# Optimization experiments

Measured on AMD Instinct MI355X. Metric: run time of the kernel, lower is better.

The kernel has to match this reference:

```python
import jax, jax.numpy as jnp
import numpy as np

N_NODES = 100000
N_EDGES = 1600000
F_IN = 128
F_OUT = 128


def _spmm(edge_row, edge_col, edge_weight, X):
    # sparse [N,N] @ dense [N,F]: gather source rows, weight, scatter-add to dest rows
    msgs = edge_weight[:, None] * X[edge_col]  # [E, F]
    return jax.ops.segment_sum(msgs, edge_row, num_segments=N_NODES)


def setup_inputs() -> dict:
    key = jax.random.key(0)
    ks = jax.random.split(key, 7)
    scale = 1.0 / np.sqrt(F_IN)
    return {
        "x": jax.random.normal(ks[0], (N_NODES, F_IN), dtype=jnp.float32),
        "edge_row": jax.random.randint(ks[1], (N_EDGES,), 0, N_NODES, dtype=jnp.int32),
        "edge_col": jax.random.randint(ks[2], (N_EDGES,), 0, N_NODES, dtype=jnp.int32),
        "edge_weight": jax.random.uniform(ks[3], (N_EDGES,), dtype=jnp.float32),
        "w1": jax.random.normal(ks[4], (F_IN, F_IN), dtype=jnp.float32) * scale,
        "w2": jax.random.normal(ks[5], (F_IN, F_OUT), dtype=jnp.float32) * scale,
        "w3": jax.random.normal(ks[6], (F_OUT, F_OUT), dtype=jnp.float32) * scale,
    }


def reference(x, edge_row, edge_col, edge_weight, w1, w2, w3):
    # dropout p=0.0 (eval) -> identity
    h = jax.nn.relu(_spmm(edge_row, edge_col, edge_weight, x @ w1))
    h = jax.nn.relu(_spmm(edge_row, edge_col, edge_weight, h @ w2))
    h = jax.nn.relu(_spmm(edge_row, edge_col, edge_weight, h @ w3))
    return h
```

## Files before the change

### kernel.cpp

```cpp
#include <hip/hip_runtime.h>

#define N_NODES 100000
#define N_EDGES 1600000
#define F 128
#define XCD_RANGE 12500

#define SCAN_B 1024
#define SCAN_NB ((N_NODES + SCAN_B - 1) / SCAN_B)

typedef short bf16x8 __attribute__((ext_vector_type(8)));
typedef float f32x4  __attribute__((ext_vector_type(4)));
typedef unsigned int u32x4 __attribute__((ext_vector_type(4)));

union ABFrag {
    bf16x8 v;
    unsigned short u[8];
    u32x4  q;
};

__device__ __forceinline__ unsigned short f2bf(float f) {
    unsigned int u = __float_as_uint(f);
    u += 0x7fffu + ((u >> 16) & 1u);
    return (unsigned short)(u >> 16);
}
__device__ __forceinline__ float bflo(unsigned int u) {
    return __uint_as_float(u << 16);
}
__device__ __forceinline__ float bfhi(unsigned int u) {
    return __uint_as_float(u & 0xFFFF0000u);
}


__global__ __launch_bounds__(256) void edge_histogram_xcd(
    const int* __restrict__ erow, int* __restrict__ counts) {
    const int xcd = blockIdx.x & 7;
    const int e   = (blockIdx.x >> 3) * 256 + threadIdx.x;
    const int dst = erow[e];
    const int lo  = xcd * XCD_RANGE;
    if (dst >= lo && dst < lo + XCD_RANGE) {
        atomicAdd(&counts[dst], 1);
    }
}

__global__ void scan_block_sums(const int* __restrict__ counts, int* __restrict__ bsums) {
    __shared__ int s[SCAN_B];
    const int t = threadIdx.x;
    const int idx = blockIdx.x * SCAN_B + t;
    int v = (idx < N_NODES) ? counts[idx] : 0;
    s[t] = v;
    __syncthreads();
    for (int off = SCAN_B / 2; off > 0; off >>= 1) {
        if (t < off) s[t] += s[t + off];
        __syncthreads();
    }
    if (t == 0) bsums[blockIdx.x] = s[0];
}

__global__ void scan_bsums(const int* __restrict__ bsums, int* __restrict__ boffs) {
    __shared__ int s[128];
    const int t = threadIdx.x;
    int v = (t < SCAN_NB) ? bsums[t] : 0;
    s[t] = v;
    __syncthreads();
    for (int off = 1; off < 128; off <<= 1) {
        int u = (t >= off) ? s[t - off] : 0;
        __syncthreads();
        s[t] += u;
        __syncthreads();
    }
    if (t < SCAN_NB) boffs[t] = s[t] - v;
}

__global__ void scan_final(const int* __restrict__ counts, const int* __restrict__ boffs,
                           int* __restrict__ row_ptr) {
    __shared__ int s[SCAN_B];
    const int t = threadIdx.x;
    const int idx = blockIdx.x * SCAN_B + t;
    int v = (idx < N_NODES) ? counts[idx] : 0;
    s[t] = v;
    __syncthreads();
    for (int off = 1; off < SCAN_B; off <<= 1) {
        int u = (t >= off) ? s[t - off] : 0;
        __syncthreads();
        s[t] += u;
        __syncthreads();
    }
    if (idx < N_NODES) row_ptr[idx] = boffs[blockIdx.x] + s[t] - v;
    if (idx == 0) row_ptr[N_NODES] = N_EDGES;
}

__global__ __launch_bounds__(256) void csr_fill_xcd(
    const int* __restrict__ erow, const int* __restrict__ ecol,
    const float* __restrict__ ewgt,
    const int* __restrict__ row_ptr, int* __restrict__ cursor,
    unsigned int* __restrict__ pairs) {
    const int xcd = blockIdx.x & 7;
    const int e   = (blockIdx.x >> 3) * 256 + threadIdx.x;
    const int dst = erow[e];
    const int lo  = xcd * XCD_RANGE;
    if (dst >= lo && dst < lo + XCD_RANGE) {
        const int col = ecol[e];
        const float w = ewgt[e];
        const int pos = atomicAdd(&cursor[dst], 1);
        pairs[row_ptr[dst] + pos] = ((unsigned int)col << 15) | (unsigned int)f2bf(w);
    }
}

__global__ void transpose_w3(const float* __restrict__ w1, const float* __restrict__ w2,
                             const float* __restrict__ w3, unsigned short* __restrict__ wt) {
    const int i = blockIdx.x * 256 + threadIdx.x;
    const int which = i >> 14;
    const int j = i & 16383;
    const float* W = (which == 0) ? w1 : (which == 1) ? w2 : w3;
    const int n = j >> 7;
    const int k = j & 127;
    wt[i] = f2bf(W[k * F + n]);
}

__global__ __launch_bounds__(256) void gemm_mfma(
    const float* __restrict__ Xf,
    const unsigned short* __restrict__ Xb,
    const unsigned short* __restrict__ Wt,
    unsigned short* __restrict__ Y,
    int use_f32_in)
{
    __shared__ unsigned short Wl[4 * 8 * 64 * 8];

    const int tid  = threadIdx.x;
    const int wave = tid >> 6;
    const int lane = tid & 63;

    for (int s = tid; s < 2048; s += 256) {
        const int ln  = s & 63;
        const int ntk = s >> 6;
        const int nt  = ntk & 7;
        const int kt  = ntk >> 3;
        const int n   = nt * 16 + (ln & 15);
        const int k   = kt * 32 + (ln >> 4) * 8;
        *(u32x4*)(&Wl[s * 8]) = *(const u32x4*)(Wt + n * F + k);
    }
    __syncthreads();

    const int kq = (lane >> 4) * 8;
    const int m0 = blockIdx.x * 128 + wave * 16 + (lane & 15);
    const int m1 = m0 + 64;
    const bool v0 = (m0 < N_NODES);
    const bool v1 = (m1 < N_NODES);

    f32x4 acc[2][8] = {};

#pragma unroll
    for (int kt = 0; kt < 4; ++kt) {
        ABFrag a0, a1;
        a0.q = 0;
        a1.q = 0;
        if (use_f32_in) {
            if (v0) {
                const float* p = Xf + (size_t)m0 * F + kt * 32 + kq;
                const float4 u0 = *(const float4*)p;
                const float4 u1 = *(const float4*)(p + 4);
                a0.u[0] = f2bf(u0.x); a0.u[1] = f2bf(u0.y);
                a0.u[2] = f2bf(u0.z); a0.u[3] = f2bf(u0.w);
                a0.u[4] = f2bf(u1.x); a0.u[5] = f2bf(u1.y);
                a0.u[6] = f2bf(u1.z); a0.u[7] = f2bf(u1.w);
            }
            if (v1) {
                const float* p = Xf + (size_t)m1 * F + kt * 32 + kq;
                const float4 u0 = *(const float4*)p;
                const float4 u1 = *(const float4*)(p + 4);
                a1.u[0] = f2bf(u0.x); a1.u[1] = f2bf(u0.y);
                a1.u[2] = f2bf(u0.z); a1.u[3] = f2bf(u0.w);
                a1.u[4] = f2bf(u1.x); a1.u[5] = f2bf(u1.y);
                a1.u[6] = f2bf(u1.z); a1.u[7] = f2bf(u1.w);
            }
        } else {
            if (v0) {
                a0.q = *(const u32x4*)(Xb + (size_t)m0 * F + kt * 32 + kq);
#pragma unroll
                for (int j = 0; j < 8; ++j)
                    if (a0.u[j] & 0x8000u) a0.u[j] = 0;
            }
            if (v1) {
                a1.q = *(const u32x4*)(Xb + (size_t)m1 * F + kt * 32 + kq);
#pragma unroll
                for (int j = 0; j < 8; ++j)
                    if (a1.u[j] & 0x8000u) a1.u[j] = 0;
            }
        }
#pragma unroll
        for (int nt = 0; nt < 8; ++nt) {
            ABFrag b;
            b.q = *(const u32x4*)(&Wl[((kt * 8 + nt) * 64 + lane) * 8]);
            acc[0][nt] = __builtin_amdgcn_mfma_f32_16x16x32_bf16(a0.v, b.v, acc[0][nt], 0, 0, 0);
            acc[1][nt] = __builtin_amdgcn_mfma_f32_16x16x32_bf16(a1.v, b.v, acc[1][nt], 0, 0, 0);
        }
    }

    const int cbase = lane & 15;
#pragma unroll
    for (int t = 0; t < 2; ++t) {
        const int rbase = blockIdx.x * 128 + t * 64 + wave * 16 + (lane >> 4) * 4;
#pragma unroll
        for (int r = 0; r < 4; ++r) {
            const int row = rbase + r;
            if (row < N_NODES) {
#pragma unroll
                for (int nt = 0; nt < 8; ++nt) {
                    Y[(size_t)row * F + nt * 16 + cbase] = f2bf(acc[t][nt][r]);
                }
            }
        }
    }
}

__global__ __launch_bounds__(256) void spmm_csr_bf16(
    const unsigned short* __restrict__ Xb,
    const int* __restrict__ row_ptr,
    const unsigned int* __restrict__ pairs,
    unsigned short* __restrict__ Ob,
    float* __restrict__ Of,
    int final_mode) {
    const int tid = threadIdx.x;
    const int l16 = tid & 15;
    const int q   = tid >> 4;
    const int row = blockIdx.x * 16 + q;

    const int beg = row_ptr[row];
    const int end = row_ptr[row + 1];

    float a[8] = {};
    int i = beg;
    for (; i + 3 < end; i += 4) {
        const unsigned int p0 = __builtin_nontemporal_load(&pairs[i]);
        const unsigned int p1 = __builtin_nontemporal_load(&pairs[i + 1]);
        const unsigned int p2 = __builtin_nontemporal_load(&pairs[i + 2]);
        const unsigned int p3 = __builtin_nontemporal_load(&pairs[i + 3]);
        const u32x4 v0 = *(const u32x4*)(Xb + (size_t)(p0 >> 15) * F + l16 * 8);
        const u32x4 v1 = *(const u32x4*)(Xb + (size_t)(p1 >> 15) * F + l16 * 8);
        const u32x4 v2 = *(const u32x4*)(Xb + (size_t)(p2 >> 15) * F + l16 * 8);
        const u32x4 v3 = *(const u32x4*)(Xb + (size_t)(p3 >> 15) * F + l16 * 8);
        const float w0 = bflo(p0 & 0x7FFFu);
        const float w1 = bflo(p1 & 0x7FFFu);
        const float w2 = bflo(p2 & 0x7FFFu);
        const float w3 = bflo(p3 & 0x7FFFu);
        a[0] += w0 * bflo(v0.x); a[1] += w0 * bfhi(v0.x);
        a[2] += w0 * bflo(v0.y); a[3] += w0 * bfhi(v0.y);
        a[4] += w0 * bflo(v0.z); a[5] += w0 * bfhi(v0.z);
        a[6] += w0 * bflo(v0.w); a[7] += w0 * bfhi(v0.w);
        a[0] += w1 * bflo(v1.x); a[1] += w1 * bfhi(v1.x);
        a[2] += w1 * bflo(v1.y); a[3] += w1 * bfhi(v1.y);
        a[4] += w1 * bflo(v1.z); a[5] += w1 * bfhi(v1.z);
        a[6] += w1 * bflo(v1.w); a[7] += w1 * bfhi(v1.w);
        a[0] += w2 * bflo(v2.x); a[1] += w2 * bfhi(v2.x);
        a[2] += w2 * bflo(v2.y); a[3] += w2 * bfhi(v2.y);
        a[4] += w2 * bflo(v2.z); a[5] += w2 * bfhi(v2.z);
        a[6] += w2 * bflo(v2.w); a[7] += w2 * bfhi(v2.w);
        a[0] += w3 * bflo(v3.x); a[1] += w3 * bfhi(v3.x);
        a[2] += w3 * bflo(v3.y); a[3] += w3 * bfhi(v3.y);
        a[4] += w3 * bflo(v3.z); a[5] += w3 * bfhi(v3.z);
        a[6] += w3 * bflo(v3.w); a[7] += w3 * bfhi(v3.w);
    }
    for (; i < end; ++i) {
        const unsigned int p0 = __builtin_nontemporal_load(&pairs[i]);
        const u32x4 v0 = *(const u32x4*)(Xb + (size_t)(p0 >> 15) * F + l16 * 8);
        const float w0 = bflo(p0 & 0x7FFFu);
        a[0] += w0 * bflo(v0.x); a[1] += w0 * bfhi(v0.x);
        a[2] += w0 * bflo(v0.y); a[3] += w0 * bfhi(v0.y);
        a[4] += w0 * bflo(v0.z); a[5] += w0 * bfhi(v0.z);
        a[6] += w0 * bflo(v0.w); a[7] += w0 * bfhi(v0.w);
    }

    if (final_mode) {
        f32x4 o0 = {fmaxf(a[0], 0.f), fmaxf(a[1], 0.f), fmaxf(a[2], 0.f), fmaxf(a[3], 0.f)};
        f32x4 o1 = {fmaxf(a[4], 0.f), fmaxf(a[5], 0.f), fmaxf(a[6], 0.f), fmaxf(a[7], 0.f)};
        float* p = Of + (size_t)row * F + l16 * 8;
        __builtin_nontemporal_store(o0, (f32x4*)p);
        __builtin_nontemporal_store(o1, (f32x4*)(p + 4));
    } else {
        u32x4 o;
        o.x = (unsigned int)f2bf(a[0]) | ((unsigned int)f2bf(a[1]) << 16);
        o.y = (unsigned int)f2bf(a[2]) | ((unsigned int)f2bf(a[3]) << 16);
        o.z = (unsigned int)f2bf(a[4]) | ((unsigned int)f2bf(a[5]) << 16);
        o.w = (unsigned int)f2bf(a[6]) | ((unsigned int)f2bf(a[7]) << 16);
        __builtin_nontemporal_store(o, (u32x4*)(Ob + (size_t)row * F + l16 * 8));
    }
}


extern "C" void kernel_launch(void* const* d_in, const int* in_sizes, int n_in,
                              void* d_out, int out_size, void* d_ws, size_t ws_size,
                              hipStream_t stream) {
    const float* x    = (const float*)d_in[0];
    const int*   erow = (const int*)d_in[1];
    const int*   ecol = (const int*)d_in[2];
    const float* ew   = (const float*)d_in[3];
    const float* w1   = (const float*)d_in[4];
    const float* w2   = (const float*)d_in[5];
    const float* w3   = (const float*)d_in[6];
    float* out = (float*)d_out;

    char* ws = (char*)d_ws;
    size_t off = 0;
    auto alloc = [&](size_t bytes) -> char* {
        char* p = ws + off;
        off += (bytes + 255) & ~(size_t)255;
        return p;
    };
    unsigned short* bufA = (unsigned short*)alloc((size_t)N_NODES * F * 2);
    unsigned short* bufB = (unsigned short*)alloc((size_t)N_NODES * F * 2);
    unsigned int* pairs  = (unsigned int*)alloc((size_t)N_EDGES * 4);
    int* counts  = (int*)alloc((size_t)N_NODES * sizeof(int) * 2);
    int* cursor  = counts + N_NODES;
    int* row_ptr = (int*)alloc(((size_t)N_NODES + 1) * sizeof(int));
    int* bsums   = (int*)alloc((size_t)SCAN_NB * sizeof(int));
    int* boffs   = (int*)alloc((size_t)SCAN_NB * sizeof(int));
    unsigned short* wt = (unsigned short*)alloc((size_t)3 * F * F * 2);
    unsigned short* wt1 = wt;
    unsigned short* wt2 = wt + F * F;
    unsigned short* wt3 = wt + 2 * F * F;

    hipMemsetAsync(counts, 0, (size_t)N_NODES * sizeof(int) * 2, stream);
    edge_histogram_xcd<<<8 * (N_EDGES / 256), 256, 0, stream>>>(erow, counts);
    scan_block_sums<<<SCAN_NB, SCAN_B, 0, stream>>>(counts, bsums);
    scan_bsums<<<1, 128, 0, stream>>>(bsums, boffs);
    scan_final<<<SCAN_NB, SCAN_B, 0, stream>>>(counts, boffs, row_ptr);
    csr_fill_xcd<<<8 * (N_EDGES / 256), 256, 0, stream>>>(erow, ecol, ew, row_ptr, cursor, pairs);

    transpose_w3<<<192, 256, 0, stream>>>(w1, w2, w3, wt);

    const int ggrid = (N_NODES + 127) / 128;
    const int sgrid = N_NODES / 16;

    gemm_mfma<<<ggrid, 256, 0, stream>>>(x, nullptr, wt1, bufA, 1);
    spmm_csr_bf16<<<sgrid, 256, 0, stream>>>(bufA, row_ptr, pairs, bufB, nullptr, 0);
    gemm_mfma<<<ggrid, 256, 0, stream>>>(nullptr, bufB, wt2, bufA, 0);
    spmm_csr_bf16<<<sgrid, 256, 0, stream>>>(bufA, row_ptr, pairs, bufB, nullptr, 0);
    gemm_mfma<<<ggrid, 256, 0, stream>>>(nullptr, bufB, wt3, bufA, 0);
    spmm_csr_bf16<<<sgrid, 256, 0, stream>>>(bufA, row_ptr, pairs, nullptr, out, 1);
}
```

Baseline: 509.1 us.

## Stage GEMM output through LDS for coalesced stores, simplify histogram

Result: no change. 512.4 us (+0.6%).

```diff
diff --git a/kernel.cpp b/kernel.cpp
--- a/kernel.cpp
+++ b/kernel.cpp
@@ -31,15 +31,10 @@
 }
 
 
-__global__ __launch_bounds__(256) void edge_histogram_xcd(
+__global__ __launch_bounds__(256) void edge_histogram(
     const int* __restrict__ erow, int* __restrict__ counts) {
-    const int xcd = blockIdx.x & 7;
-    const int e   = (blockIdx.x >> 3) * 256 + threadIdx.x;
-    const int dst = erow[e];
-    const int lo  = xcd * XCD_RANGE;
-    if (dst >= lo && dst < lo + XCD_RANGE) {
-        atomicAdd(&counts[dst], 1);
-    }
+    const int e = blockIdx.x * blockDim.x + threadIdx.x;
+    atomicAdd(&counts[__builtin_nontemporal_load(&erow[e])], 1);
 }
 
 __global__ void scan_block_sums(const int* __restrict__ counts, int* __restrict__ bsums) {
@@ -96,11 +91,11 @@
     unsigned int* __restrict__ pairs) {
     const int xcd = blockIdx.x & 7;
     const int e   = (blockIdx.x >> 3) * 256 + threadIdx.x;
-    const int dst = erow[e];
+    const int dst = __builtin_nontemporal_load(&erow[e]);
     const int lo  = xcd * XCD_RANGE;
     if (dst >= lo && dst < lo + XCD_RANGE) {
-        const int col = ecol[e];
-        const float w = ewgt[e];
+        const int col = __builtin_nontemporal_load(&ecol[e]);
+        const float w = __builtin_nontemporal_load(&ewgt[e]);
         const int pos = atomicAdd(&cursor[dst], 1);
         pairs[row_ptr[dst] + pos] = ((unsigned int)col << 15) | (unsigned int)f2bf(w);
     }
@@ -117,6 +112,7 @@
     wt[i] = f2bf(W[k * F + n]);
 }
 
+#define LDS_PITCH 136
 __global__ __launch_bounds__(256) void gemm_mfma(
     const float* __restrict__ Xf,
     const unsigned short* __restrict__ Xb,
@@ -124,7 +120,7 @@
     unsigned short* __restrict__ Y,
     int use_f32_in)
 {
-    __shared__ unsigned short Wl[4 * 8 * 64 * 8];
+    __shared__ unsigned short Lds[128 * LDS_PITCH];
 
     const int tid  = threadIdx.x;
     const int wave = tid >> 6;
@@ -137,7 +133,7 @@
         const int kt  = ntk >> 3;
         const int n   = nt * 16 + (ln & 15);
         const int k   = kt * 32 + (ln >> 4) * 8;
-        *(u32x4*)(&Wl[s * 8]) = *(const u32x4*)(Wt + n * F + k);
+        *(u32x4*)(&Lds[s * 8]) = *(const u32x4*)(Wt + n * F + k);
     }
     __syncthreads();
 
@@ -190,25 +186,35 @@
 #pragma unroll
         for (int nt = 0; nt < 8; ++nt) {
             ABFrag b;
-            b.q = *(const u32x4*)(&Wl[((kt * 8 + nt) * 64 + lane) * 8]);
+            b.q = *(const u32x4*)(&Lds[((kt * 8 + nt) * 64 + lane) * 8]);
             acc[0][nt] = __builtin_amdgcn_mfma_f32_16x16x32_bf16(a0.v, b.v, acc[0][nt], 0, 0, 0);
             acc[1][nt] = __builtin_amdgcn_mfma_f32_16x16x32_bf16(a1.v, b.v, acc[1][nt], 0, 0, 0);
         }
     }
 
-    const int cbase = lane & 15;
+    __syncthreads();
+    const int cb = lane & 15;
 #pragma unroll
     for (int t = 0; t < 2; ++t) {
-        const int rbase = blockIdx.x * 128 + t * 64 + wave * 16 + (lane >> 4) * 4;
+        const int rl = t * 64 + wave * 16 + ((lane >> 4) << 2);
 #pragma unroll
         for (int r = 0; r < 4; ++r) {
-            const int row = rbase + r;
-            if (row < N_NODES) {
-#pragma unroll
-                for (int nt = 0; nt < 8; ++nt) {
-                    Y[(size_t)row * F + nt * 16 + cbase] = f2bf(acc[t][nt][r]);
-                }
-            }
+#pragma unroll
+            for (int nt = 0; nt < 8; ++nt) {
+                Lds[(rl + r) * LDS_PITCH + nt * 16 + cb] = f2bf(acc[t][nt][r]);
+            }
+        }
+    }
+    __syncthreads();
+    const int rowBase = blockIdx.x * 128;
+#pragma unroll
+    for (int i = tid; i < 2048; i += 256) {
+        const int lr = i >> 4;
+        const int ch = i & 15;
+        const int row = rowBase + lr;
+        if (row < N_NODES) {
+            u32x4 v = *(const u32x4*)(&Lds[lr * LDS_PITCH + ch * 8]);
+            *(u32x4*)(Y + (size_t)row * F + ch * 8) = v;
         }
     }
 }
@@ -320,7 +326,7 @@
     unsigned short* wt3 = wt + 2 * F * F;
 
     hipMemsetAsync(counts, 0, (size_t)N_NODES * sizeof(int) * 2, stream);
-    edge_histogram_xcd<<<8 * (N_EDGES / 256), 256, 0, stream>>>(erow, counts);
+    edge_histogram<<<N_EDGES / 256, 256, 0, stream>>>(erow, counts);
     scan_block_sums<<<SCAN_NB, SCAN_B, 0, stream>>>(counts, bsums);
     scan_bsums<<<1, 128, 0, stream>>>(bsums, boffs);
     scan_final<<<SCAN_NB, SCAN_B, 0, stream>>>(counts, boffs, row_ptr);
```
